# Kernel tuning notes

Hardware: AMD Instinct MI355X
Metric: run time of the kernel (lower is better)

Reference implementation:

```python
import jax, jax.numpy as jnp
import numpy as np

T = 0.5  # moco temperature


def _normalize(x, axis):
    return x / jnp.clip(jnp.linalg.norm(x, axis=axis, keepdims=True), 1e-12)


def _balanced_bce(logits, labels):
    # BalancedCrossEntropyLoss(size_average=True): class-frequency weighted BCE-with-logits
    numel = labels.size
    num_pos = jnp.sum(labels)
    num_neg = numel - num_pos
    loss = jax.nn.softplus(-logits) * labels + jax.nn.softplus(logits) * (1.0 - labels)
    loss_pos = jnp.sum(labels * loss)
    loss_neg = jnp.sum((1.0 - labels) * loss)
    return ((num_neg / numel) * loss_pos + (num_pos / numel) * loss_neg) / numel


def setup_inputs() -> dict:
    key = jax.random.key(0)
    ks = jax.random.split(key, 4)
    B, D, H, W, K = 8, 32, 48, 48, 8192
    return {
        "q_feat": jax.random.normal(ks[0], (B, D, H, W), jnp.float32),
        "k_feat": jax.random.normal(ks[1], (B, D, H, W), jnp.float32),
        "q_bg": jax.random.normal(ks[2], (B, H, W), jnp.float32),
        "sal_q": jnp.ones((B, H, W), jnp.float32),
        "sal_k": jnp.ones((B, H, W), jnp.float32),
        "queue": jax.random.normal(ks[3], (32, K), jnp.float32),
        "num_negatives": 5,
    }


def reference(q_feat, k_feat, q_bg, sal_q, sal_k, queue, num_negatives):
    B, D, H, W = q_feat.shape
    HW = H * W
    key = jax.random.key(42)
    k_dir, k_neg = jax.random.split(key)

    # q = normalize(model_q(im_q))
    qn = _normalize(q_feat, axis=1)                            # (B,D,H,W)
    q_flat = qn.transpose(0, 2, 3, 1).reshape(-1, D)           # (B*HW, D)
    sal_loss = _balanced_bce(q_bg, sal_q)

    # batch-id per foreground pixel; with all-ones sal every pixel is foreground
    offset = jnp.arange(0, 2 * B, 2, dtype=sal_q.dtype)
    tmpv = ((sal_q + offset[:, None, None]) * sal_q).reshape(-1)
    mask_indexes = jnp.arange(B * HW)                          # nonzero() under ones-mask
    tmp = jnp.floor_divide(tmpv[mask_indexes], 2.0)

    # prototypes from key encoder (no-grad in original)
    kn = _normalize(k_feat, axis=1).reshape(B, D, HW)
    protos = jnp.einsum('bdh,bh->bd', kn, sal_k.reshape(B, HW).astype(k_feat.dtype))
    protos = _normalize(protos, axis=1)                        # (B,D)

    # random-walk positive: rejection-sampling over 4-neighborhood == uniform over
    # in-bounds neighbors; sample with masked Gumbel-argmax
    steps = jnp.array([[1, 0], [-1, 0], [0, 1], [0, -1]])
    rr, cc = jnp.meshgrid(jnp.arange(H), jnp.arange(W), indexing='ij')
    nr = rr[:, :, None] + steps[:, 0]
    nc = cc[:, :, None] + steps[:, 1]
    valid = (nr >= 0) & (nr < H) & (nc >= 0) & (nc < W)        # (H,W,4)
    g = jax.random.gumbel(k_dir, (B, H, W, 4))
    d = jnp.argmax(jnp.where(valid[None], 0.0, -jnp.inf) + g, axis=-1)  # (B,H,W)
    pr = rr[None] + steps[d, 0]
    pc = cc[None] + steps[d, 1]
    pos_idx = (pr * W + pc).reshape(B, HW)
    q_hw = qn.reshape(B, D, HW).transpose(0, 2, 1)             # (B,HW,D)
    neigh = jnp.take_along_axis(q_hw, pos_idx[:, :, None], axis=1)
    positive = jnp.sum(q_hw * neigh, axis=-1)                  # (B,HW)

    # negatives: torch.multinomial(uniform w/ self zeroed, 5, without replacement)
    # == Gumbel top-k over HW with the self index masked out
    gn = jax.random.gumbel(k_neg, (B, HW, HW))
    gn = jnp.where(jnp.eye(HW, dtype=bool)[None], -jnp.inf, gn)
    _, neg_idx = jax.lax.top_k(gn, num_negatives)              # (B,HW,nn)
    neg = q_hw[jnp.arange(B)[:, None, None], neg_idx]          # (B,HW,nn,D)
    neg_logits = jnp.einsum('bhd,bhkd->bhk', q_hw, neg)

    l_logits = jnp.concatenate([positive[..., None], neg_logits], axis=-1)
    l_logits = l_logits.reshape(B * HW, num_negatives + 1) / T
    l_labels = jnp.zeros(B * HW, jnp.float32)

    # q = index_select(q_flat, mask_indexes)  (computed but unused in original)
    _ = q_flat[mask_indexes]

    queue_n = _normalize(queue, axis=0)                        # buffer normalized at init
    l_batch = q_flat @ protos.T                                # (B*HW, B)
    l_mem = q_flat @ queue_n                                   # (B*HW, K)
    logits = jnp.concatenate([l_batch, l_mem], axis=1) / T
    return logits, tmp, l_logits, l_labels, sal_loss
```

## Files before the change

kernel.cpp:

```cpp
#include <hip/hip_runtime.h>
#include <stdint.h>

#define BB 8
#define DD 32
#define HH 48
#define WW 48
#define HWSZ 2304
#define NROW 18432
#define KQ 8192
#define NCOL 8200

#define OFF_TMP    151142400
#define OFF_LLOG   151160832
#define OFF_LLBL   151271424
#define OFF_SAL    151289856

#define N_MAIN2  5760

typedef short short8v __attribute__((ext_vector_type(8)));
typedef float float4v __attribute__((ext_vector_type(4)));

__device__ __forceinline__ uint32_t rotl_d(uint32_t x, int d){ return (x<<d)|(x>>(32-d)); }

__device__ __forceinline__ void tf2x32(uint32_t k0, uint32_t k1, uint32_t x0, uint32_t x1,
                                       uint32_t &o0, uint32_t &o1){
  uint32_t ks2 = k0 ^ k1 ^ 0x1BD11BDAu;
  x0 += k0; x1 += k1;
  x0+=x1; x1=rotl_d(x1,13); x1^=x0;
  x0+=x1; x1=rotl_d(x1,15); x1^=x0;
  x0+=x1; x1=rotl_d(x1,26); x1^=x0;
  x0+=x1; x1=rotl_d(x1, 6); x1^=x0;
  x0+=k1; x1+=ks2+1u;
  x0+=x1; x1=rotl_d(x1,17); x1^=x0;
  x0+=x1; x1=rotl_d(x1,29); x1^=x0;
  x0+=x1; x1=rotl_d(x1,16); x1^=x0;
  x0+=x1; x1=rotl_d(x1,24); x1^=x0;
  x0+=ks2; x1+=k0+2u;
  x0+=x1; x1=rotl_d(x1,13); x1^=x0;
  x0+=x1; x1=rotl_d(x1,15); x1^=x0;
  x0+=x1; x1=rotl_d(x1,26); x1^=x0;
  x0+=x1; x1=rotl_d(x1, 6); x1^=x0;
  x0+=k0; x1+=k1+3u;
  x0+=x1; x1=rotl_d(x1,17); x1^=x0;
  x0+=x1; x1=rotl_d(x1,29); x1^=x0;
  x0+=x1; x1=rotl_d(x1,16); x1^=x0;
  x0+=x1; x1=rotl_d(x1,24); x1^=x0;
  x0+=k1; x1+=ks2+4u;
  x0+=x1; x1=rotl_d(x1,13); x1^=x0;
  x0+=x1; x1=rotl_d(x1,15); x1^=x0;
  x0+=x1; x1=rotl_d(x1,26); x1^=x0;
  x0+=x1; x1=rotl_d(x1, 6); x1^=x0;
  x0+=ks2; x1+=k0+5u;
  o0=x0; o1=x1;
}

static inline uint32_t rotl_h(uint32_t x,int d){return (x<<d)|(x>>(32-d));}
static void tf_host(uint32_t k0,uint32_t k1,uint32_t x0,uint32_t x1,uint32_t&o0,uint32_t&o1){
  uint32_t ks2=k0^k1^0x1BD11BDAu;
  x0+=k0;x1+=k1;
  const int RA[4]={13,15,26,6}, RBR[4]={17,29,16,24};
  for(int i=0;i<4;++i){x0+=x1;x1=rotl_h(x1,RA[i]);x1^=x0;}
  x0+=k1; x1+=ks2+1u;
  for(int i=0;i<4;++i){x0+=x1;x1=rotl_h(x1,RBR[i]);x1^=x0;}
  x0+=ks2; x1+=k0+2u;
  for(int i=0;i<4;++i){x0+=x1;x1=rotl_h(x1,RA[i]);x1^=x0;}
  x0+=k0; x1+=k1+3u;
  for(int i=0;i<4;++i){x0+=x1;x1=rotl_h(x1,RBR[i]);x1^=x0;}
  x0+=k1; x1+=ks2+4u;
  for(int i=0;i<4;++i){x0+=x1;x1=rotl_h(x1,RA[i]);x1^=x0;}
  x0+=ks2; x1+=k0+5u;
  o0=x0;o1=x1;
}

__device__ __forceinline__ ushort f2bf(float x){
  uint32_t u = __float_as_uint(x);
  uint32_t r = (u + 0x7FFFu + ((u>>16)&1u)) >> 16;
  return (ushort)r;
}

__global__ __launch_bounds__(256) void k_pre(const float* __restrict__ q_feat,
                                             const float* __restrict__ k_feat,
                                             const float* __restrict__ q_bg,
                                             const float* __restrict__ sal_q,
                                             const float* __restrict__ sal_k,
                                             const float* __restrict__ queue,
                                             float* __restrict__ q_flat,
                                             ushort* __restrict__ qbf,
                                             ushort* __restrict__ qnT,
                                             float* __restrict__ w,
                                             float* __restrict__ tmp_out,
                                             float* __restrict__ lbl_out,
                                             float* __restrict__ acc){
  int bid = blockIdx.x;
  if (bid < 72){
    int b = bid / 9;
    int hw = (bid % 9)*256 + threadIdx.x;
    const float* src = q_feat + (size_t)b*DD*HWSZ + hw;
    float v[32]; float ss = 0.f;
#pragma unroll
    for (int d=0; d<32; ++d){ v[d] = src[(size_t)d*HWSZ]; ss += v[d]*v[d]; }
    float inv = 1.f / fmaxf(sqrtf(ss), 1e-12f);
    size_t row = (size_t)b*HWSZ + hw;
    float4* o4 = (float4*)(q_flat + row*DD);
#pragma unroll
    for (int i=0;i<8;++i)
      o4[i] = make_float4(v[4*i]*inv, v[4*i+1]*inv, v[4*i+2]*inv, v[4*i+3]*inv);
    ushort us[32];
#pragma unroll
    for (int d=0; d<32; ++d) us[d] = f2bf(v[d]*inv);
    short8v* ob = (short8v*)(qbf + row*DD);
#pragma unroll
    for (int i=0;i<4;++i) ob[i] = *(short8v*)&us[8*i];
  } else if (bid < 144){
    int rb = bid - 72;
    int b = rb / 9;
    int hw = (rb % 9)*256 + threadIdx.x;
    const float* src = k_feat + (size_t)b*DD*HWSZ + hw;
    float ss = 0.f;
#pragma unroll
    for (int d=0; d<32; ++d){ float v = src[(size_t)d*HWSZ]; ss += v*v; }
    size_t row = (size_t)b*HWSZ + hw;
    w[row] = sal_k[row] * (1.f / fmaxf(sqrtf(ss), 1e-12f));
  } else if (bid < 176){
    int j = (bid-144)*256 + threadIdx.x;
    float v[32]; float ss = 0.f;
#pragma unroll
    for (int d=0; d<DD; ++d){ v[d] = queue[(size_t)d*KQ + j]; ss += v[d]*v[d]; }
    float inv = 1.f / fmaxf(sqrtf(ss), 1e-12f);
    ushort us[32];
#pragma unroll
    for (int d=0; d<DD; ++d) us[d] = f2bf(v[d]*inv);
    short8v* ob = (short8v*)(qnT + (size_t)j*DD);
#pragma unroll
    for (int i=0;i<4;++i) ob[i] = *(short8v*)&us[8*i];
  } else {
    int i = (bid-176)*256 + threadIdx.x;
    float s = sal_q[i];
    int b = i / HWSZ;
    float tmpv = (s + 2.f*(float)b) * s;
    tmp_out[i] = floorf(tmpv * 0.5f);
    lbl_out[i] = 0.f;
    float x = q_bg[i];
    float c = log1pf(expf(-fabsf(x)));
    float sp_neg = fmaxf(-x,0.f) + c;
    float sp_pos = fmaxf( x,0.f) + c;
    float loss = sp_neg*s + sp_pos*(1.f - s);
    float a0 = s, a1 = s*loss, a2 = (1.f-s)*loss;
    a0+=__shfl_xor(a0,32,64); a1+=__shfl_xor(a1,32,64); a2+=__shfl_xor(a2,32,64);
    a0+=__shfl_xor(a0,16,64); a1+=__shfl_xor(a1,16,64); a2+=__shfl_xor(a2,16,64);
    a0+=__shfl_xor(a0, 8,64); a1+=__shfl_xor(a1, 8,64); a2+=__shfl_xor(a2, 8,64);
    a0+=__shfl_xor(a0, 4,64); a1+=__shfl_xor(a1, 4,64); a2+=__shfl_xor(a2, 4,64);
    a0+=__shfl_xor(a0, 2,64); a1+=__shfl_xor(a1, 2,64); a2+=__shfl_xor(a2, 2,64);
    a0+=__shfl_xor(a0, 1,64); a1+=__shfl_xor(a1, 1,64); a2+=__shfl_xor(a2, 1,64);
    if ((threadIdx.x&63)==0){ atomicAdd(&acc[0],a0); atomicAdd(&acc[1],a1); atomicAdd(&acc[2],a2); }
  }
}

__global__ __launch_bounds__(256) void k_protos(const float* __restrict__ kf, const float* __restrict__ w,
                                                float* __restrict__ praw){
  int bd = blockIdx.x;
  int b = bd >> 5;
  const float* src = kf + (size_t)bd*HWSZ;
  const float* wp  = w + (size_t)b*HWSZ;
  float s = 0.f;
  for (int i = threadIdx.x; i < HWSZ; i += 256) s += src[i]*wp[i];
  s += __shfl_xor(s,32,64); s+=__shfl_xor(s,16,64); s+=__shfl_xor(s,8,64);
  s+=__shfl_xor(s,4,64); s+=__shfl_xor(s,2,64); s+=__shfl_xor(s,1,64);
  __shared__ float red[4];
  int wave = threadIdx.x>>6, lane = threadIdx.x&63;
  if (lane==0) red[wave]=s;
  __syncthreads();
  if (threadIdx.x==0) praw[bd] = red[0]+red[1]+red[2]+red[3];
}

__global__ __launch_bounds__(256) void k_pnormfin(const float* __restrict__ praw, float* __restrict__ pn,
                                                  const float* __restrict__ acc, float* __restrict__ out_sal){
  int t = threadIdx.x;
  float v = praw[t];
  float ss = v*v;
  ss += __shfl_xor(ss,16,64); ss+=__shfl_xor(ss,8,64); ss+=__shfl_xor(ss,4,64);
  ss+=__shfl_xor(ss,2,64); ss+=__shfl_xor(ss,1,64);
  pn[t] = v / fmaxf(sqrtf(ss), 1e-12f);
  if (t == 0){
    float numel = (float)NROW;
    float npos = acc[0];
    float nneg = numel - npos;
    out_sal[0] = (nneg/numel*acc[1] + npos/numel*acc[2]) / numel;
  }
}

__global__ __launch_bounds__(256) void k_main(const float* __restrict__ q_flat,
                                              const ushort* __restrict__ qbf,
                                              const ushort* __restrict__ qnT,
                                              const float* __restrict__ pn,
                                              float* __restrict__ out,
                                              float* __restrict__ llog,
                                              uint32_t kd0, uint32_t kd1,
                                              uint32_t kn0, uint32_t kn1){
  __shared__ float lds[16*260];
  int bid = blockIdx.x;
  int wave = threadIdx.x>>6, lane = threadIdx.x&63;

  if ((bid % 5) == 0){
    int g = bid/5;
    int rowbase = g*16;
    int r16 = lane&15, hi = lane>>4, koff = hi*8;

    const short8v a = *(const short8v*)(qbf + ((size_t)(rowbase + r16))*DD + koff);

    if (threadIdx.x < 32){
      int row = threadIdx.x >> 1, c0 = (threadIdx.x & 1)*4;
      const float* qr = q_flat + (size_t)(rowbase+row)*DD;
      float s0=0.f,s1=0.f,s2=0.f,s3=0.f;
#pragma unroll
      for (int d=0; d<32; ++d){
        float qd = qr[d];
        s0 += qd*pn[(c0+0)*32+d];
        s1 += qd*pn[(c0+1)*32+d];
        s2 += qd*pn[(c0+2)*32+d];
        s3 += qd*pn[(c0+3)*32+d];
      }
      *(float4*)(out + (size_t)(rowbase+row)*NCOL + c0) =
          make_float4(2.f*s0, 2.f*s1, 2.f*s2, 2.f*s3);
    }

    for (int c=0; c<32; ++c){
#pragma unroll
      for (int t=0; t<4; ++t){
        int j0 = c*256 + wave*64 + t*16;
        const short8v bfr = *(const short8v*)(qnT + ((size_t)(j0 + r16))*DD + koff);
        float4v acc = {0.f,0.f,0.f,0.f};
        acc = __builtin_amdgcn_mfma_f32_16x16x32_bf16(a, bfr, acc, 0, 0, 0);
        int ccol = wave*64 + t*16 + r16;
#pragma unroll
        for (int i=0;i<4;++i) lds[(hi*4+i)*260 + ccol] = 2.f*acc[i];
      }
      __syncthreads();
#pragma unroll
      for (int k=0;k<4;++k){
        int f = threadIdx.x + k*256;
        int row = f>>6, col4 = f&63;
        float4 v = *(const float4*)&lds[row*260 + col4*4];
        *(float4*)(out + (size_t)(rowbase+row)*NCOL + 8 + c*256 + col4*4) = v;
      }
      __syncthreads();
    }
  } else {
    int l = bid - bid/5 - 1;
    int row = l*4 + wave;
    int b = row/HWSZ, h = row%HWSZ;
    int r = h/WW, c0 = h%WW;

    uint32_t m = 0;
    if (lane < 4){
      uint32_t i = (uint32_t)row*4u + (uint32_t)lane;
      uint32_t o0,o1;
      tf2x32(kd0,kd1,0u,i,o0,o1);
      m = (o0 ^ o1) >> 9;
    }
    uint32_t mm[4];
    mm[0]=__shfl(m,0,64); mm[1]=__shfl(m,1,64); mm[2]=__shfl(m,2,64); mm[3]=__shfl(m,3,64);
    const int sr[4]={1,-1,0,0}, sc[4]={0,0,1,-1};
    int best=-1; uint32_t bv=0;
#pragma unroll
    for (int j=0;j<4;++j){
      int nr=r+sr[j], nc=c0+sc[j];
      bool ok = (nr>=0)&&(nr<HH)&&(nc>=0)&&(nc<WW);
      if (ok && (best<0 || mm[j]>bv)){ best=j; bv=mm[j]; }
    }
    int pos = (r+sr[best])*WW + (c0+sc[best]);
    int prow = b*HWSZ + pos;

    float qv = 0.f, pv = 0.f;
    if (lane<32){ qv=q_flat[(size_t)row*DD+lane]; pv=q_flat[(size_t)prow*DD+lane]; }
    float d = qv*pv;
    d+=__shfl_xor(d,16,64); d+=__shfl_xor(d,8,64); d+=__shfl_xor(d,4,64);
    d+=__shfl_xor(d,2,64); d+=__shfl_xor(d,1,64);
    if (lane==0) llog[(size_t)row*6] = 2.f*d;

    uint32_t base = (uint32_t)row * (uint32_t)HWSZ + (uint32_t)lane;
    uint32_t t0=0,t1=0,t2=0,t3=0,t4=0;
#pragma unroll 4
    for (int it=0; it<36; ++it){
      uint32_t o0,o1;
      tf2x32(kn0,kn1,0u, base + (uint32_t)(it<<6), o0,o1);
      int c = lane + (it<<6);
      uint32_t key = (((o0^o1)>>3)&0xFFFFFFC0u) | (uint32_t)(35-it);
      key = (c != h) ? key : 0u;
      uint32_t mx, mn;
      mx = t0>key?t0:key; mn = t0>key?key:t0; t0=mx; key=mn;
      mx = t1>key?t1:key; mn = t1>key?key:t1; t1=mx; key=mn;
      mx = t2>key?t2:key; mn = t2>key?key:t2; t2=mx; key=mn;
      mx = t3>key?t3:key; mn = t3>key?key:t3; t3=mx; key=mn;
      t4 = t4>key?t4:key;
    }
    int idx[5];
#pragma unroll
    for (int k=0;k<5;++k){
      uint32_t mk = t0>>6;
      int it = 35 - (int)(t0 & 63u);
      int c  = lane + (it<<6);
      unsigned long long bk = ((unsigned long long)mk<<18)
                            | ((unsigned long long)(2303-c)<<6)
                            | (unsigned long long)lane;
      #pragma unroll
      for (int o=1;o<64;o<<=1){
        unsigned long long other = __shfl_xor(bk,o,64);
        if (other > bk) bk = other;
      }
      int wl = (int)(bk & 63ull);
      idx[k] = 2303 - (int)((bk >> 6) & 0xFFFull);
      if (lane == wl){ t0=t1; t1=t2; t2=t3; t3=t4; t4=0; }
    }
#pragma unroll
    for (int k=0;k<5;++k){
      float nv = 0.f;
      if (lane < 32) nv = q_flat[(size_t)(b*HWSZ + idx[k])*DD + lane];
      float dd = qv*nv;
      dd+=__shfl_xor(dd,16,64); dd+=__shfl_xor(dd,8,64); dd+=__shfl_xor(dd,4,64);
      dd+=__shfl_xor(dd,2,64); dd+=__shfl_xor(dd,1,64);
      if (lane==0) llog[(size_t)row*6 + 1 + k] = 2.f*dd;
    }
  }
}

extern "C" void kernel_launch(void* const* d_in, const int* in_sizes, int n_in,
                              void* d_out, int out_size, void* d_ws, size_t ws_size,
                              hipStream_t stream) {
  const float* q_feat = (const float*)d_in[0];
  const float* k_feat = (const float*)d_in[1];
  const float* q_bg   = (const float*)d_in[2];
  const float* sal_q  = (const float*)d_in[3];
  const float* sal_k  = (const float*)d_in[4];
  const float* queue  = (const float*)d_in[5];
  (void)in_sizes; (void)n_in; (void)out_size; (void)ws_size;

  float* out    = (float*)d_out;
  float* logits = out;
  float* tmp    = out + OFF_TMP;
  float* llog   = out + OFF_LLOG;
  float* llbl   = out + OFF_LLBL;
  float* sal    = out + OFF_SAL;

  float* ws     = (float*)d_ws;
  float*  q_flat = ws;
  ushort* qbf    = (ushort*)(ws + 589824);
  ushort* qnT    = (ushort*)(ws + 884736);
  float*  wk     = ws + 1015808;
  float*  praw   = ws + 1034240;
  float*  pn     = ws + 1034496;
  float*  acc    = ws + 1034752;

  uint32_t kd0,kd1,kn0,kn1;
  tf_host(0u,42u,0u,0u,kd0,kd1);
  tf_host(0u,42u,0u,1u,kn0,kn1);

  hipMemsetAsync(acc, 0, 3*sizeof(float), stream);

  k_pre     <<<248, 256, 0, stream>>>(q_feat, k_feat, q_bg, sal_q, sal_k, queue,
                                      q_flat, qbf, qnT, wk, tmp, llbl, acc);
  k_protos  <<<256, 256, 0, stream>>>(k_feat, wk, praw);
  k_pnormfin<<<1,   256, 0, stream>>>(praw, pn, acc, sal);
  k_main    <<<N_MAIN2, 256, 0, stream>>>(q_flat, qbf, qnT, pn, logits, llog,
                                          kd0, kd1, kn0, kn1);
}
```

Measured before the change: 207.1 us.

## Fuse prototype reduction into k_pre and use nontemporal stores for outputs

The k_feat normalization blocks now also compute the weighted prototype sums directly. They keep the loaded values in registers, reduce across each wave with shuffles, combine in shared memory and atomically add into praw. This removes the separate k_protos kernel and its second read of k_feat. Large logits and tmp/label output writes switch to nontemporal stores to reduce cache pollution. Float atomics make the prototype sums order-nondeterministic, and the memset is widened to zero praw and acc together.

```diff
diff --git a/kernel.cpp b/kernel.cpp
--- a/kernel.cpp
+++ b/kernel.cpp
@@ -87,10 +87,11 @@
                                              float* __restrict__ q_flat,
                                              ushort* __restrict__ qbf,
                                              ushort* __restrict__ qnT,
-                                             float* __restrict__ w,
+                                             float* __restrict__ praw,
                                              float* __restrict__ tmp_out,
                                              float* __restrict__ lbl_out,
                                              float* __restrict__ acc){
+  __shared__ float pacc[32];
   int bid = blockIdx.x;
   if (bid < 72){
     int b = bid / 9;
@@ -116,11 +117,22 @@
     int b = rb / 9;
     int hw = (rb % 9)*256 + threadIdx.x;
     const float* src = k_feat + (size_t)b*DD*HWSZ + hw;
-    float ss = 0.f;
-#pragma unroll
-    for (int d=0; d<32; ++d){ float v = src[(size_t)d*HWSZ]; ss += v*v; }
-    size_t row = (size_t)b*HWSZ + hw;
-    w[row] = sal_k[row] * (1.f / fmaxf(sqrtf(ss), 1e-12f));
+    float v[32]; float ss = 0.f;
+#pragma unroll
+    for (int d=0; d<32; ++d){ v[d] = src[(size_t)d*HWSZ]; ss += v[d]*v[d]; }
+    float w_t = sal_k[(size_t)b*HWSZ + hw] * (1.f / fmaxf(sqrtf(ss), 1e-12f));
+    if (threadIdx.x < 32) pacc[threadIdx.x] = 0.f;
+    __syncthreads();
+    int lane = threadIdx.x & 63;
+#pragma unroll
+    for (int d=0; d<32; ++d){
+      float s = v[d]*w_t;
+      s+=__shfl_xor(s,32,64); s+=__shfl_xor(s,16,64); s+=__shfl_xor(s,8,64);
+      s+=__shfl_xor(s,4,64);  s+=__shfl_xor(s,2,64);  s+=__shfl_xor(s,1,64);
+      if (lane==0) atomicAdd(&pacc[d], s);
+    }
+    __syncthreads();
+    if (threadIdx.x < 32) atomicAdd(&praw[b*32 + threadIdx.x], pacc[threadIdx.x]);
   } else if (bid < 176){
     int j = (bid-144)*256 + threadIdx.x;
     float v[32]; float ss = 0.f;
@@ -138,8 +150,8 @@
     float s = sal_q[i];
     int b = i / HWSZ;
     float tmpv = (s + 2.f*(float)b) * s;
-    tmp_out[i] = floorf(tmpv * 0.5f);
-    lbl_out[i] = 0.f;
+    __builtin_nontemporal_store(floorf(tmpv * 0.5f), &tmp_out[i]);
+    __builtin_nontemporal_store(0.f, &lbl_out[i]);
     float x = q_bg[i];
     float c = log1pf(expf(-fabsf(x)));
     float sp_neg = fmaxf(-x,0.f) + c;
@@ -156,23 +168,6 @@
   }
 }
 
-__global__ __launch_bounds__(256) void k_protos(const float* __restrict__ kf, const float* __restrict__ w,
-                                                float* __restrict__ praw){
-  int bd = blockIdx.x;
-  int b = bd >> 5;
-  const float* src = kf + (size_t)bd*HWSZ;
-  const float* wp  = w + (size_t)b*HWSZ;
-  float s = 0.f;
-  for (int i = threadIdx.x; i < HWSZ; i += 256) s += src[i]*wp[i];
-  s += __shfl_xor(s,32,64); s+=__shfl_xor(s,16,64); s+=__shfl_xor(s,8,64);
-  s+=__shfl_xor(s,4,64); s+=__shfl_xor(s,2,64); s+=__shfl_xor(s,1,64);
-  __shared__ float red[4];
-  int wave = threadIdx.x>>6, lane = threadIdx.x&63;
-  if (lane==0) red[wave]=s;
-  __syncthreads();
-  if (threadIdx.x==0) praw[bd] = red[0]+red[1]+red[2]+red[3];
-}
-
 __global__ __launch_bounds__(256) void k_pnormfin(const float* __restrict__ praw, float* __restrict__ pn,
                                                   const float* __restrict__ acc, float* __restrict__ out_sal){
   int t = threadIdx.x;
@@ -220,8 +215,9 @@
         s2 += qd*pn[(c0+2)*32+d];
         s3 += qd*pn[(c0+3)*32+d];
       }
-      *(float4*)(out + (size_t)(rowbase+row)*NCOL + c0) =
-          make_float4(2.f*s0, 2.f*s1, 2.f*s2, 2.f*s3);
+      float4v hv = {2.f*s0, 2.f*s1, 2.f*s2, 2.f*s3};
+      __builtin_nontemporal_store(hv,
+          (float4v*)(out + (size_t)(rowbase+row)*NCOL + c0));
     }
 
     for (int c=0; c<32; ++c){
@@ -240,8 +236,9 @@
       for (int k=0;k<4;++k){
         int f = threadIdx.x + k*256;
         int row = f>>6, col4 = f&63;
-        float4 v = *(const float4*)&lds[row*260 + col4*4];
-        *(float4*)(out + (size_t)(rowbase+row)*NCOL + 8 + c*256 + col4*4) = v;
+        float4v v = *(const float4v*)&lds[row*260 + col4*4];
+        __builtin_nontemporal_store(v,
+            (float4v*)(out + (size_t)(rowbase+row)*NCOL + 8 + c*256 + col4*4));
       }
       __syncthreads();
     }
@@ -346,20 +343,18 @@
   float*  q_flat = ws;
   ushort* qbf    = (ushort*)(ws + 589824);
   ushort* qnT    = (ushort*)(ws + 884736);
-  float*  wk     = ws + 1015808;
-  float*  praw   = ws + 1034240;
-  float*  pn     = ws + 1034496;
-  float*  acc    = ws + 1034752;
+  float*  praw   = ws + 1015808;
+  float*  acc    = ws + 1016064;
+  float*  pn     = ws + 1016128;
 
   uint32_t kd0,kd1,kn0,kn1;
   tf_host(0u,42u,0u,0u,kd0,kd1);
   tf_host(0u,42u,0u,1u,kn0,kn1);
 
-  hipMemsetAsync(acc, 0, 3*sizeof(float), stream);
+  (void)hipMemsetAsync(praw, 0, 259*sizeof(float), stream);
 
   k_pre     <<<248, 256, 0, stream>>>(q_feat, k_feat, q_bg, sal_q, sal_k, queue,
-                                      q_flat, qbf, qnT, wk, tmp, llbl, acc);
-  k_protos  <<<256, 256, 0, stream>>>(k_feat, wk, praw);
+                                      q_flat, qbf, qnT, praw, tmp, llbl, acc);
   k_pnormfin<<<1,   256, 0, stream>>>(praw, pn, acc, sal);
   k_main    <<<N_MAIN2, 256, 0, stream>>>(q_flat, qbf, qnT, pn, logits, llog,
                                           kd0, kd1, kn0, kn1);
```

Measured after the change: 190.8 us. 7.9% less time.
